# Performance work log

Measured on AMD Instinct MI355X. Metric: run time of the kernel, lower is better.

Reference implementation:

```python
import jax, jax.numpy as jnp
import numpy as np

BITS = 4
GROUP_SIZE = 128
INF, OUTF, TOKENS = 4096, 11008, 256


def setup_inputs() -> dict:
    key = jax.random.key(0)
    k1, k2, k3, k4, k5 = jax.random.split(key, 5)
    n_groups = INF // GROUP_SIZE  # 32
    x = jax.random.normal(k1, (TOKENS, INF), dtype=jnp.float32)
    qweight = jax.random.randint(k2, (INF // 32 * BITS, OUTF), 0, 2**31 - 1, dtype=jnp.int32)
    qzeros = jax.random.randint(k3, (n_groups, OUTF // 32 * BITS), 0, 2**31 - 1, dtype=jnp.int32)
    scales = jax.random.uniform(k4, (n_groups, OUTF), dtype=jnp.float32, minval=1e-3, maxval=2e-2)
    bias = jax.random.normal(k5, (OUTF,), dtype=jnp.float32)
    return {"x": x, "qweight": qweight, "qzeros": qzeros, "scales": scales, "bias": bias}


def _dequantize(qweight, qzeros, scales):
    """Unpack int4 nibbles and build the fp32 weight [infeatures, outfeatures]."""
    shifts = jnp.arange(0, 32, BITS, dtype=jnp.int32)  # [8]
    mask = (1 << BITS) - 1
    out_f = qweight.shape[1]
    # qweight row packs 8 consecutive in-features -> [K, O] int in [0, 15]
    w = ((qweight[:, None, :] >> shifts[None, :, None]) & mask).reshape(-1, out_f)
    # qzeros col packs 8 consecutive out-features; stored as (zero - 1)
    n_groups = qzeros.shape[0]
    z = (((qzeros[:, :, None] >> shifts[None, None, :]) & mask) + 1).reshape(n_groups, out_f)
    g_idx = jnp.arange(w.shape[0], dtype=jnp.int32) // GROUP_SIZE  # [K]
    return (w - z[g_idx]).astype(jnp.float32) * scales[g_idx]


def reference(x, qweight, qzeros, scales, bias):
    W = _dequantize(qweight, qzeros, scales)  # [infeatures, outfeatures]
    return x @ W + bias  # [tokens, outfeatures]
```

## Files before the change

### kernel.cpp

```cpp
#include <hip/hip_runtime.h>
#include <stdint.h>

#define TOKENS  256
#define INF     4096
#define OUTF    11008
#define NGROUPS 32
#define NPHASE  16
#define NTH     256

typedef __attribute__((ext_vector_type(2))) _Float16 f16x2;
typedef __attribute__((ext_vector_type(8))) _Float16 f16x8;
typedef __attribute__((ext_vector_type(2))) __fp16   pkh2;
typedef __attribute__((ext_vector_type(4))) float    f32x4;

union U32H2 { uint32_t u; f16x2 h; };
union H8    { f16x2 h2[4]; f16x8 h8; };
union PK    { pkh2 p; f16x2 h; };

__device__ __forceinline__ void gl2lds16(const void* g, void* l) {
    __builtin_amdgcn_global_load_lds(
        (const __attribute__((address_space(1))) uint32_t*)g,
        (__attribute__((address_space(3))) uint32_t*)l, 16, 0, 0);
}

__device__ __forceinline__ int Fswz(int m4) {
    return (m4 & 0xF) | (((m4 ^ (m4 >> 1)) & 1) << 4);
}

__global__ __launch_bounds__(NTH)
void cvt_x(const float* __restrict__ x, _Float16* __restrict__ x16) {
    const int t   = blockIdx.x * NTH + threadIdx.x;
    const int row = t >> 9;
    const int c   = t & 511;
    const float* p = x + (size_t)row * INF + c * 8;
    f32x4 v0 = *(const f32x4*)p;
    f32x4 v1 = *(const f32x4*)(p + 4);
    H8 o; PK k0, k1, k2, k3;
    k0.p = __builtin_amdgcn_cvt_pkrtz(v0[0], v1[0]);
    k1.p = __builtin_amdgcn_cvt_pkrtz(v0[1], v1[1]);
    k2.p = __builtin_amdgcn_cvt_pkrtz(v0[2], v1[2]);
    k3.p = __builtin_amdgcn_cvt_pkrtz(v0[3], v1[3]);
    o.h2[0] = k0.h; o.h2[1] = k1.h; o.h2[2] = k2.h; o.h2[3] = k3.h;
    *(f16x8*)(x16 + (size_t)row * INF + c * 8) = o.h8;
}

__global__ __launch_bounds__(NTH, 2)
void qlin_main(const _Float16* __restrict__ x16,
               const uint32_t* __restrict__ qweight,
               const uint32_t* __restrict__ qzeros,
               const float* __restrict__ scales,
               const float* __restrict__ bias,
               float* __restrict__ out)
{
    __shared__ alignas(16) _Float16 As[2][64 * 256];

    const int tid = threadIdx.x;
    const int bx  = blockIdx.x >> 2;
    const int by  = blockIdx.x & 3;

    const int lane = tid & 63;
    const int quad = lane >> 4;
    const int l16  = lane & 15;
    const int wv   = tid >> 6;

    const int rowoff = (tid >> 5) & 7;
    const int sclin  = tid & 31;
    const int row0   = by * 64;
    const uint32_t aoffE = (uint32_t)((row0 + rowoff)     * (INF * 2) + (sclin ^ Fswz(rowoff))     * 16);
    const uint32_t aoffO = (uint32_t)((row0 + 8 + rowoff) * (INF * 2) + (sclin ^ Fswz(8 + rowoff)) * 16);
    const char* x16b = (const char*)x16;
    _Float16* ldsW = &As[0][0];
    const int ldsSlotBase = wv * 512;

    const int col0 = bx * 128 + wv * 32 + l16;
    const int col1 = col0 + 16;
    const int bOff0 = quad * OUTF + col0;
    const int bOff1 = quad * OUTF + col1;
    const int zsh = (col0 & 7) * 4;

    const int fsw = Fswz(l16);

    f32x4 acc[4][2];
#pragma unroll
    for (int mi = 0; mi < 4; ++mi)
#pragma unroll
        for (int nf = 0; nf < 2; ++nf)
            acc[mi][nf] = f32x4{0.f, 0.f, 0.f, 0.f};

    uint32_t Breg[2][16];
    float    sS[2][4];
    uint32_t qZ[2][4];

#pragma unroll
    for (int ii = 0; ii < 4; ++ii) {
        gl2lds16(x16b + aoffE + ii * 131072, ldsW + (2 * ii)     * 2048 + ldsSlotBase);
        gl2lds16(x16b + aoffO + ii * 131072, ldsW + (2 * ii + 1) * 2048 + ldsSlotBase);
    }
#pragma unroll
    for (int s = 0; s < 8; ++s) {
        const uint32_t* qp = qweight + (size_t)(s * 4) * OUTF;
        Breg[0][2 * s + 0] = qp[bOff0];
        Breg[0][2 * s + 1] = qp[bOff1];
    }
    sS[0][0] = scales[0 * OUTF + col0]; sS[0][1] = scales[0 * OUTF + col1];
    sS[0][2] = scales[1 * OUTF + col0]; sS[0][3] = scales[1 * OUTF + col1];
    qZ[0][0] = qzeros[0 * (OUTF / 8) + (col0 >> 3)]; qZ[0][1] = qzeros[0 * (OUTF / 8) + (col1 >> 3)];
    qZ[0][2] = qzeros[1 * (OUTF / 8) + (col0 >> 3)]; qZ[0][3] = qzeros[1 * (OUTF / 8) + (col1 >> 3)];
    __syncthreads();

#define PHASE_BODY(PAR, P, DO_PREFETCH)                                          \
    {                                                                            \
        const int p_ = (P);                                                      \
        if (DO_PREFETCH) {                                                       \
            const int pn = p_ + 1;                                               \
            const uint32_t pb = (uint32_t)(pn * 512);                            \
            _Float16* ldsN = ldsW + (1 - (PAR)) * 16384;                         \
            _Pragma("unroll")                                                    \
            for (int ii = 0; ii < 4; ++ii) {                                     \
                gl2lds16(x16b + aoffE + ii * 131072 + pb,                        \
                         ldsN + (2 * ii)     * 2048 + ldsSlotBase);              \
                gl2lds16(x16b + aoffO + ii * 131072 + pb,                        \
                         ldsN + (2 * ii + 1) * 2048 + ldsSlotBase);              \
            }                                                                    \
            const uint32_t* qpb = qweight + (size_t)(pn * 32) * OUTF;            \
            _Pragma("unroll")                                                    \
            for (int s = 0; s < 8; ++s) {                                        \
                const uint32_t* qp = qpb + (size_t)(s * 4) * OUTF;               \
                Breg[1 - (PAR)][2 * s + 0] = qp[bOff0];                          \
                Breg[1 - (PAR)][2 * s + 1] = qp[bOff1];                          \
            }                                                                    \
            const int g0 = 2 * pn, g1 = 2 * pn + 1;                              \
            sS[1 - (PAR)][0] = scales[g0 * OUTF + col0];                         \
            sS[1 - (PAR)][1] = scales[g0 * OUTF + col1];                         \
            sS[1 - (PAR)][2] = scales[g1 * OUTF + col0];                         \
            sS[1 - (PAR)][3] = scales[g1 * OUTF + col1];                         \
            qZ[1 - (PAR)][0] = qzeros[g0 * (OUTF / 8) + (col0 >> 3)];            \
            qZ[1 - (PAR)][1] = qzeros[g0 * (OUTF / 8) + (col1 >> 3)];            \
            qZ[1 - (PAR)][2] = qzeros[g1 * (OUTF / 8) + (col0 >> 3)];            \
            qZ[1 - (PAR)][3] = qzeros[g1 * (OUTF / 8) + (col1 >> 3)];            \
        }                                                                        \
        f16x2 hs2[2][2], hz2[2][2];                                              \
        _Pragma("unroll")                                                        \
        for (int gh = 0; gh < 2; ++gh)                                           \
            _Pragma("unroll")                                                    \
            for (int nf = 0; nf < 2; ++nf) {                                     \
                const float s = sS[PAR][gh * 2 + nf];                            \
                const int   z = (int)((qZ[PAR][gh * 2 + nf] >> zsh) & 15u) + 1025; \
                const _Float16 hs = (_Float16)s;                                 \
                const _Float16 hz = (_Float16)(-(float)z);                       \
                hs2[gh][nf] = f16x2{hs, hs};                                     \
                hz2[gh][nf] = f16x2{hz, hz};                                     \
            }                                                                    \
        const _Float16* buf = ldsW + (PAR) * 16384;                              \
        _Pragma("unroll")                                                        \
        for (int s = 0; s < 8; ++s) {                                            \
            const int gh = s >> 2;                                               \
            f16x8 af[4];                                                         \
            _Pragma("unroll")                                                    \
            for (int mi = 0; mi < 4; ++mi) {                                     \
                const int m  = mi * 16 + l16;                                    \
                const int sc = (s * 4 + quad) ^ fsw;                             \
                af[mi] = *(const f16x8*)(buf + m * 256 + sc * 8);                \
            }                                                                    \
            _Pragma("unroll")                                                    \
            for (int nf = 0; nf < 2; ++nf) {                                     \
                const uint32_t q = Breg[PAR][2 * s + nf];                        \
                H8 b;                                                            \
                _Pragma("unroll")                                                \
                for (int j = 0; j < 4; ++j) {                                    \
                    U32H2 u;                                                     \
                    u.u = ((q >> (4 * j)) & 0x000F000Fu) | 0x64006400u;          \
                    b.h2[j] = (u.h + hz2[gh][nf]) * hs2[gh][nf];                 \
                }                                                                \
                _Pragma("unroll")                                                \
                for (int mi = 0; mi < 4; ++mi)                                   \
                    acc[mi][nf] = __builtin_amdgcn_mfma_f32_16x16x32_f16(        \
                        af[mi], b.h8, acc[mi][nf], 0, 0, 0);                     \
            }                                                                    \
        }                                                                        \
        __syncthreads();                                                         \
    }

#pragma unroll 1
    for (int pp = 0; pp < NPHASE / 2; ++pp) {
        PHASE_BODY(0, 2 * pp, true)
        PHASE_BODY(1, 2 * pp + 1, (pp < NPHASE / 2 - 1))
    }
#undef PHASE_BODY

#pragma unroll
    for (int nf = 0; nf < 2; ++nf) {
        const int col = (nf == 0) ? col0 : col1;
        const float bv = bias[col];
#pragma unroll
        for (int mi = 0; mi < 4; ++mi) {
            const int r0 = by * 64 + mi * 16 + quad * 4;
#pragma unroll
            for (int rg = 0; rg < 4; ++rg)
                out[(size_t)(r0 + rg) * OUTF + col] = acc[mi][nf][rg] + bv;
        }
    }
}

__global__ __launch_bounds__(NTH, 2)
void qlin_fb(const float* __restrict__ x,
             const uint32_t* __restrict__ qweight,
             const uint32_t* __restrict__ qzeros,
             const float* __restrict__ scales,
             const float* __restrict__ bias,
             float* __restrict__ out)
{
    __shared__ alignas(16) _Float16 Asb[64][40];
    __shared__ alignas(16) _Float16 Bsb[128][40];
    const int tid = threadIdx.x;
    const int bx = blockIdx.x, by = blockIdx.y;
    const int am = tid >> 2, ar = tid & 3;
    const float* xrow = x + (size_t)(by * 64 + am) * INF + ar * 8;
    const int bc = tid & 127, br = tid >> 7;
    const int bn = bx * 128 + bc;
    const int bswz = (bc >> 3) & 3;
    const int lane = tid & 63, quad = lane >> 4, l16 = lane & 15;
    const int wv = tid >> 6, wm = wv >> 1, wn = wv & 1;
    f32x4 acc[2][4];
#pragma unroll
    for (int i = 0; i < 2; ++i)
#pragma unroll
        for (int j = 0; j < 4; ++j) acc[i][j] = f32x4{0.f, 0.f, 0.f, 0.f};
    f32x4 pa0 = *(const f32x4*)(xrow + 0);
    f32x4 pa1 = *(const f32x4*)(xrow + 4);
    uint32_t pq0 = qweight[(size_t)br * OUTF + bn];
    uint32_t pq1 = qweight[(size_t)(br + 2) * OUTF + bn];
    for (int g = 0; g < NGROUPS; ++g) {
        const float s = scales[g * OUTF + bn];
        const uint32_t qzv = qzeros[g * (OUTF / 8) + (bn >> 3)];
        const int z = (int)((qzv >> (4 * (bn & 7))) & 15u) + 1;
        const _Float16 hs = (_Float16)s;
        const _Float16 hz = (_Float16)(-(float)(1024 + z));
        const f16x2 hs2 = {hs, hs}, hz2 = {hz, hz};
#pragma unroll
        for (int t4 = 0; t4 < 4; ++t4) {
            const int it = (g << 2) + t4;
            { H8 ah; PK p0, p1, p2, p3;
              p0.p = __builtin_amdgcn_cvt_pkrtz(pa0[0], pa1[0]);
              p1.p = __builtin_amdgcn_cvt_pkrtz(pa0[1], pa1[1]);
              p2.p = __builtin_amdgcn_cvt_pkrtz(pa0[2], pa1[2]);
              p3.p = __builtin_amdgcn_cvt_pkrtz(pa0[3], pa1[3]);
              ah.h2[0] = p0.h; ah.h2[1] = p1.h; ah.h2[2] = p2.h; ah.h2[3] = p3.h;
              *(f16x8*)&Asb[am][ar * 8] = ah.h8; }
            { const uint32_t qq[2] = {pq0, pq1};
#pragma unroll
              for (int rr = 0; rr < 2; ++rr) {
                  const int r = br + rr * 2; H8 bh;
#pragma unroll
                  for (int jp = 0; jp < 4; ++jp) {
                      U32H2 u; u.u = ((qq[rr] >> (4 * jp)) & 0x000F000Fu) | 0x64006400u;
                      bh.h2[jp] = (u.h + hz2) * hs2;
                  }
                  *(f16x8*)&Bsb[bc][(r ^ bswz) * 8] = bh.h8;
              } }
            __syncthreads();
            const int itn = (it < 127) ? it + 1 : 127;
            pa0 = *(const f32x4*)(xrow + itn * 32);
            pa1 = *(const f32x4*)(xrow + itn * 32 + 4);
            pq0 = qweight[(size_t)(itn * 4 + br) * OUTF + bn];
            pq1 = qweight[(size_t)(itn * 4 + br + 2) * OUTF + bn];
            f16x8 af[2], bf[4];
#pragma unroll
            for (int mi = 0; mi < 2; ++mi)
                af[mi] = *(const f16x8*)&Asb[wm * 32 + mi * 16 + l16][quad * 8];
#pragma unroll
            for (int ni = 0; ni < 4; ++ni) {
                const int c = wn * 64 + ni * 16 + l16;
                bf[ni] = *(const f16x8*)&Bsb[c][(quad ^ ((c >> 3) & 3)) * 8];
            }
#pragma unroll
            for (int mi = 0; mi < 2; ++mi)
#pragma unroll
                for (int ni = 0; ni < 4; ++ni)
                    acc[mi][ni] = __builtin_amdgcn_mfma_f32_16x16x32_f16(
                        af[mi], bf[ni], acc[mi][ni], 0, 0, 0);
            __syncthreads();
        }
    }
#pragma unroll
    for (int ni = 0; ni < 4; ++ni) {
        const int col = bx * 128 + wn * 64 + ni * 16 + l16;
        const float bv = bias[col];
#pragma unroll
        for (int mi = 0; mi < 2; ++mi) {
            const int row0 = by * 64 + wm * 32 + mi * 16 + quad * 4;
#pragma unroll
            for (int rg = 0; rg < 4; ++rg)
                out[(size_t)(row0 + rg) * OUTF + col] = acc[mi][ni][rg] + bv;
        }
    }
}

extern "C" void kernel_launch(void* const* d_in, const int* in_sizes, int n_in,
                              void* d_out, int out_size, void* d_ws, size_t ws_size,
                              hipStream_t stream) {
    const float*    xx = (const float*)d_in[0];
    const uint32_t* qw = (const uint32_t*)d_in[1];
    const uint32_t* qz = (const uint32_t*)d_in[2];
    const float*    sc = (const float*)d_in[3];
    const float*    bs = (const float*)d_in[4];
    float* out = (float*)d_out;

    const size_t x16_bytes = (size_t)TOKENS * INF * sizeof(_Float16);
    if (ws_size >= x16_bytes) {
        _Float16* x16 = (_Float16*)d_ws;
        cvt_x<<<(TOKENS * INF / 8) / NTH, NTH, 0, stream>>>(xx, x16);
        qlin_main<<<(OUTF / 128) * (TOKENS / 64), NTH, 0, stream>>>(x16, qw, qz, sc, bs, out);
    } else {
        dim3 grid(OUTF / 128, TOKENS / 64);
        qlin_fb<<<grid, NTH, 0, stream>>>(xx, qw, qz, sc, bs, out);
    }
}
```

Before: 122.3 us.

## Split K in two with atomic accumulation and bias pre-initialized output

Splits the K dimension across two blocks, doubling the grid from 344 to 688 blocks, and accumulates partial results into the output with float atomics. A new kernel first fills the output with the bias. The per-phase K tile shrinks to 128 with a simpler XOR swizzle, and LDS use halves so occupancy can rise to three blocks per CU. Block indices are remapped so that blocks sharing a weight strip run close together in time. The aim is to fill more CUs on a GEMM that was short of blocks. The cost is an extra launch, atomic traffic on the output, and a summation order that is no longer deterministic.

```diff
diff --git a/kernel.cpp b/kernel.cpp
--- a/kernel.cpp
+++ b/kernel.cpp
@@ -5,7 +5,9 @@
 #define INF     4096
 #define OUTF    11008
 #define NGROUPS 32
-#define NPHASE  16
+#define KSPLIT  2
+#define PHK     128
+#define NPH     ((INF / KSPLIT) / PHK)
 #define NTH     256
 
 typedef __attribute__((ext_vector_type(2))) _Float16 f16x2;
@@ -21,10 +23,6 @@
     __builtin_amdgcn_global_load_lds(
         (const __attribute__((address_space(1))) uint32_t*)g,
         (__attribute__((address_space(3))) uint32_t*)l, 16, 0, 0);
-}
-
-__device__ __forceinline__ int Fswz(int m4) {
-    return (m4 & 0xF) | (((m4 ^ (m4 >> 1)) & 1) << 4);
 }
 
 __global__ __launch_bounds__(NTH)
@@ -44,30 +42,46 @@
     *(f16x8*)(x16 + (size_t)row * INF + c * 8) = o.h8;
 }
 
-__global__ __launch_bounds__(NTH, 2)
+__global__ __launch_bounds__(NTH)
+void init_out(const float* __restrict__ bias, float* __restrict__ out) {
+    const int t = blockIdx.x * NTH + threadIdx.x;
+    const int c = t % (OUTF / 4);
+    const int r = t / (OUTF / 4);
+    const f32x4 b = ((const f32x4*)bias)[c];
+    ((f32x4*)out)[(size_t)r * (OUTF / 4) + c] = b;
+}
+
+__global__ __launch_bounds__(NTH, 3)
 void qlin_main(const _Float16* __restrict__ x16,
                const uint32_t* __restrict__ qweight,
                const uint32_t* __restrict__ qzeros,
                const float* __restrict__ scales,
-               const float* __restrict__ bias,
                float* __restrict__ out)
 {
-    __shared__ alignas(16) _Float16 As[2][64 * 256];
+    __shared__ alignas(16) _Float16 As[2][64 * PHK];
 
     const int tid = threadIdx.x;
-    const int bx  = blockIdx.x >> 2;
-    const int by  = blockIdx.x & 3;
+
+    const int d  = blockIdx.x;
+    const int cx = d & 7, kk = d >> 3;
+    int strip, memb;
+    if (kk < 80) { strip = cx * 10 + (kk >> 3); memb = kk & 7; }
+    else         { const int t2 = ((kk - 80) << 3) | cx; strip = 80 + (t2 >> 3); memb = t2 & 7; }
+    const int bx = strip;
+    const int by = memb >> 1;
+    const int ks = memb & 1;
 
     const int lane = tid & 63;
     const int quad = lane >> 4;
     const int l16  = lane & 15;
     const int wv   = tid >> 6;
 
-    const int rowoff = (tid >> 5) & 7;
-    const int sclin  = tid & 31;
+    const int rowoff = tid >> 4;
+    const int chk    = tid & 15;
     const int row0   = by * 64;
-    const uint32_t aoffE = (uint32_t)((row0 + rowoff)     * (INF * 2) + (sclin ^ Fswz(rowoff))     * 16);
-    const uint32_t aoffO = (uint32_t)((row0 + 8 + rowoff) * (INF * 2) + (sclin ^ Fswz(8 + rowoff)) * 16);
+    const uint32_t aoff = (uint32_t)((row0 + rowoff) * (INF * 2)
+                                     + ks * (INF / KSPLIT) * 2
+                                     + ((chk ^ rowoff) & 15) * 16);
     const char* x16b = (const char*)x16;
     _Float16* ldsW = &As[0][0];
     const int ldsSlotBase = wv * 512;
@@ -76,9 +90,9 @@
     const int col1 = col0 + 16;
     const int bOff0 = quad * OUTF + col0;
     const int bOff1 = quad * OUTF + col1;
-    const int zsh = (col0 & 7) * 4;
-
-    const int fsw = Fswz(l16);
+    const int zsh   = (col0 & 7) * 4;
+    const int qrow0 = ks * (INF / KSPLIT / 8);
+    const int g0    = ks * (NGROUPS / KSPLIT);
 
     f32x4 acc[4][2];
 #pragma unroll
@@ -87,25 +101,25 @@
         for (int nf = 0; nf < 2; ++nf)
             acc[mi][nf] = f32x4{0.f, 0.f, 0.f, 0.f};
 
-    uint32_t Breg[2][16];
-    float    sS[2][4];
-    uint32_t qZ[2][4];
-
-#pragma unroll
-    for (int ii = 0; ii < 4; ++ii) {
-        gl2lds16(x16b + aoffE + ii * 131072, ldsW + (2 * ii)     * 2048 + ldsSlotBase);
-        gl2lds16(x16b + aoffO + ii * 131072, ldsW + (2 * ii + 1) * 2048 + ldsSlotBase);
-    }
-#pragma unroll
-    for (int s = 0; s < 8; ++s) {
-        const uint32_t* qp = qweight + (size_t)(s * 4) * OUTF;
-        Breg[0][2 * s + 0] = qp[bOff0];
-        Breg[0][2 * s + 1] = qp[bOff1];
-    }
-    sS[0][0] = scales[0 * OUTF + col0]; sS[0][1] = scales[0 * OUTF + col1];
-    sS[0][2] = scales[1 * OUTF + col0]; sS[0][3] = scales[1 * OUTF + col1];
-    qZ[0][0] = qzeros[0 * (OUTF / 8) + (col0 >> 3)]; qZ[0][1] = qzeros[0 * (OUTF / 8) + (col1 >> 3)];
-    qZ[0][2] = qzeros[1 * (OUTF / 8) + (col0 >> 3)]; qZ[0][3] = qzeros[1 * (OUTF / 8) + (col1 >> 3)];
+    uint32_t Breg[2][8];
+    float    sS[2][2];
+    uint32_t qZ[2][2];
+
+#pragma unroll
+    for (int r = 0; r < 4; ++r)
+        gl2lds16(x16b + aoff + r * 131072, ldsW + r * 2048 + ldsSlotBase);
+    {
+        const uint32_t* qp = qweight + (size_t)qrow0 * OUTF;
+#pragma unroll
+        for (int s = 0; s < 4; ++s) {
+            Breg[0][2 * s + 0] = qp[(size_t)(s * 4) * OUTF + bOff0];
+            Breg[0][2 * s + 1] = qp[(size_t)(s * 4) * OUTF + bOff1];
+        }
+        sS[0][0] = scales[g0 * OUTF + col0];
+        sS[0][1] = scales[g0 * OUTF + col1];
+        qZ[0][0] = qzeros[g0 * (OUTF / 8) + (col0 >> 3)];
+        qZ[0][1] = qzeros[g0 * (OUTF / 8) + (col1 >> 3)];
+    }
     __syncthreads();
 
 #define PHASE_BODY(PAR, P, DO_PREFETCH)                                          \
@@ -113,54 +127,43 @@
         const int p_ = (P);                                                      \
         if (DO_PREFETCH) {                                                       \
             const int pn = p_ + 1;                                               \
-            const uint32_t pb = (uint32_t)(pn * 512);                            \
-            _Float16* ldsN = ldsW + (1 - (PAR)) * 16384;                         \
+            const uint32_t pb = (uint32_t)(pn * (PHK * 2));                      \
+            _Float16* ldsN = ldsW + (1 - (PAR)) * 8192;                          \
             _Pragma("unroll")                                                    \
-            for (int ii = 0; ii < 4; ++ii) {                                     \
-                gl2lds16(x16b + aoffE + ii * 131072 + pb,                        \
-                         ldsN + (2 * ii)     * 2048 + ldsSlotBase);              \
-                gl2lds16(x16b + aoffO + ii * 131072 + pb,                        \
-                         ldsN + (2 * ii + 1) * 2048 + ldsSlotBase);              \
+            for (int r = 0; r < 4; ++r)                                          \
+                gl2lds16(x16b + aoff + r * 131072 + pb,                          \
+                         ldsN + r * 2048 + ldsSlotBase);                         \
+            const uint32_t* qpb = qweight + (size_t)(qrow0 + pn * 16) * OUTF;    \
+            _Pragma("unroll")                                                    \
+            for (int s = 0; s < 4; ++s) {                                        \
+                Breg[1 - (PAR)][2 * s + 0] = qpb[(size_t)(s * 4) * OUTF + bOff0];\
+                Breg[1 - (PAR)][2 * s + 1] = qpb[(size_t)(s * 4) * OUTF + bOff1];\
             }                                                                    \
-            const uint32_t* qpb = qweight + (size_t)(pn * 32) * OUTF;            \
-            _Pragma("unroll")                                                    \
-            for (int s = 0; s < 8; ++s) {                                        \
-                const uint32_t* qp = qpb + (size_t)(s * 4) * OUTF;               \
-                Breg[1 - (PAR)][2 * s + 0] = qp[bOff0];                          \
-                Breg[1 - (PAR)][2 * s + 1] = qp[bOff1];                          \
-            }                                                                    \
-            const int g0 = 2 * pn, g1 = 2 * pn + 1;                              \
-            sS[1 - (PAR)][0] = scales[g0 * OUTF + col0];                         \
-            sS[1 - (PAR)][1] = scales[g0 * OUTF + col1];                         \
-            sS[1 - (PAR)][2] = scales[g1 * OUTF + col0];                         \
-            sS[1 - (PAR)][3] = scales[g1 * OUTF + col1];                         \
-            qZ[1 - (PAR)][0] = qzeros[g0 * (OUTF / 8) + (col0 >> 3)];            \
-            qZ[1 - (PAR)][1] = qzeros[g0 * (OUTF / 8) + (col1 >> 3)];            \
-            qZ[1 - (PAR)][2] = qzeros[g1 * (OUTF / 8) + (col0 >> 3)];            \
-            qZ[1 - (PAR)][3] = qzeros[g1 * (OUTF / 8) + (col1 >> 3)];            \
+            const int gn = g0 + pn;                                              \
+            sS[1 - (PAR)][0] = scales[gn * OUTF + col0];                         \
+            sS[1 - (PAR)][1] = scales[gn * OUTF + col1];                         \
+            qZ[1 - (PAR)][0] = qzeros[gn * (OUTF / 8) + (col0 >> 3)];            \
+            qZ[1 - (PAR)][1] = qzeros[gn * (OUTF / 8) + (col1 >> 3)];            \
         }                                                                        \
-        f16x2 hs2[2][2], hz2[2][2];                                              \
+        f16x2 hs2[2], hz2[2];                                                    \
         _Pragma("unroll")                                                        \
-        for (int gh = 0; gh < 2; ++gh)                                           \
-            _Pragma("unroll")                                                    \
-            for (int nf = 0; nf < 2; ++nf) {                                     \
-                const float s = sS[PAR][gh * 2 + nf];                            \
-                const int   z = (int)((qZ[PAR][gh * 2 + nf] >> zsh) & 15u) + 1025; \
-                const _Float16 hs = (_Float16)s;                                 \
-                const _Float16 hz = (_Float16)(-(float)z);                       \
-                hs2[gh][nf] = f16x2{hs, hs};                                     \
-                hz2[gh][nf] = f16x2{hz, hz};                                     \
-            }                                                                    \
-        const _Float16* buf = ldsW + (PAR) * 16384;                              \
+        for (int nf = 0; nf < 2; ++nf) {                                         \
+            const float s = sS[PAR][nf];                                         \
+            const int   z = (int)((qZ[PAR][nf] >> zsh) & 15u) + 1025;            \
+            const _Float16 hs = (_Float16)s;                                     \
+            const _Float16 hz = (_Float16)(-(float)z);                           \
+            hs2[nf] = f16x2{hs, hs};                                             \
+            hz2[nf] = f16x2{hz, hz};                                             \
+        }                                                                        \
+        const _Float16* buf = ldsW + (PAR) * 8192;                               \
         _Pragma("unroll")                                                        \
-        for (int s = 0; s < 8; ++s) {                                            \
-            const int gh = s >> 2;                                               \
+        for (int s = 0; s < 4; ++s) {                                            \
             f16x8 af[4];                                                         \
             _Pragma("unroll")                                                    \
             for (int mi = 0; mi < 4; ++mi) {                                     \
                 const int m  = mi * 16 + l16;                                    \
-                const int sc = (s * 4 + quad) ^ fsw;                             \
-                af[mi] = *(const f16x8*)(buf + m * 256 + sc * 8);                \
+                const int sc = ((s * 4 + quad) ^ l16) & 15;                      \
+                af[mi] = *(const f16x8*)(buf + m * PHK + sc * 8);                \
             }                                                                    \
             _Pragma("unroll")                                                    \
             for (int nf = 0; nf < 2; ++nf) {                                     \
@@ -170,7 +173,7 @@
                 for (int j = 0; j < 4; ++j) {                                    \
                     U32H2 u;                                                     \
                     u.u = ((q >> (4 * j)) & 0x000F000Fu) | 0x64006400u;          \
-                    b.h2[j] = (u.h + hz2[gh][nf]) * hs2[gh][nf];                 \
+                    b.h2[j] = (u.h + hz2[nf]) * hs2[nf];                         \
                 }                                                                \
                 _Pragma("unroll")                                                \
                 for (int mi = 0; mi < 4; ++mi)                                   \
@@ -182,22 +185,22 @@
     }
 
 #pragma unroll 1
-    for (int pp = 0; pp < NPHASE / 2; ++pp) {
+    for (int pp = 0; pp < NPH / 2; ++pp) {
         PHASE_BODY(0, 2 * pp, true)
-        PHASE_BODY(1, 2 * pp + 1, (pp < NPHASE / 2 - 1))
+        PHASE_BODY(1, 2 * pp + 1, (pp < NPH / 2 - 1))
     }
 #undef PHASE_BODY
 
 #pragma unroll
     for (int nf = 0; nf < 2; ++nf) {
         const int col = (nf == 0) ? col0 : col1;
-        const float bv = bias[col];
 #pragma unroll
         for (int mi = 0; mi < 4; ++mi) {
             const int r0 = by * 64 + mi * 16 + quad * 4;
 #pragma unroll
             for (int rg = 0; rg < 4; ++rg)
-                out[(size_t)(r0 + rg) * OUTF + col] = acc[mi][nf][rg] + bv;
+                unsafeAtomicAdd(&out[(size_t)(r0 + rg) * OUTF + col],
+                                acc[mi][nf][rg]);
         }
     }
 }
@@ -309,8 +312,10 @@
     const size_t x16_bytes = (size_t)TOKENS * INF * sizeof(_Float16);
     if (ws_size >= x16_bytes) {
         _Float16* x16 = (_Float16*)d_ws;
+        init_out<<<(TOKENS * OUTF / 4) / NTH, NTH, 0, stream>>>(bs, out);
         cvt_x<<<(TOKENS * INF / 8) / NTH, NTH, 0, stream>>>(xx, x16);
-        qlin_main<<<(OUTF / 128) * (TOKENS / 64), NTH, 0, stream>>>(x16, qw, qz, sc, bs, out);
+        qlin_main<<<(OUTF / 128) * (TOKENS / 64) * KSPLIT, NTH, 0, stream>>>(
+            x16, qw, qz, sc, out);
     } else {
         dim3 grid(OUTF / 128, TOKENS / 64);
         qlin_fb<<<grid, NTH, 0, stream>>>(xx, qw, qz, sc, bs, out);
```

New measurement: 123.7 us. No clear change (+1.2%).
